# Kernel tuning notes

Measured on AMD Instinct MI355X. Metric: run time of the kernel, lower is better.

Reference implementation:

```python
import jax, jax.numpy as jnp
import numpy as np

DT = 0.03125                                   # ray-march step size
NSTEPS = int(np.ceil(2.0 * np.sqrt(3.0) / DT)) # enough steps to cross the [-1,1]^3 cube diagonal (=111)


def trilinear_sample(vol, pos):
    """vol: [C, D, Hv, Wv]; pos: [H, W, 3] xyz in [-1,1] (grid_sample convention,
    align_corners=True). Returns [C, H, W]."""
    D, Hv, Wv = vol.shape[1], vol.shape[2], vol.shape[3]

    def axis(g, n):
        g = jnp.clip((g + 1.0) * 0.5 * (n - 1), 0.0, n - 1.0)
        i0 = jnp.minimum(jnp.floor(g).astype(jnp.int32), n - 2)
        return i0, i0 + 1, (g - i0)[None]  # frac broadcast over channel dim

    x0, x1, fx = axis(pos[..., 0], Wv)
    y0, y1, fy = axis(pos[..., 1], Hv)
    z0, z1, fz = axis(pos[..., 2], D)

    def g(z, y, x):
        return vol[:, z, y, x]  # [C, H, W]

    c00 = g(z0, y0, x0) * (1 - fx) + g(z0, y0, x1) * fx
    c01 = g(z0, y1, x0) * (1 - fx) + g(z0, y1, x1) * fx
    c10 = g(z1, y0, x0) * (1 - fx) + g(z1, y0, x1) * fx
    c11 = g(z1, y1, x0) * (1 - fx) + g(z1, y1, x1) * fx
    c0 = c00 * (1 - fy) + c01 * fy
    c1 = c10 * (1 - fy) + c11 * fy
    return c0 * (1 - fz) + c1 * fz


def setup_inputs() -> dict:
    key = jax.random.key(0)
    B, H, W, D = 2, 256, 256, 128
    camrot = jnp.tile(jnp.eye(3, dtype=jnp.float32)[None], (B, 1, 1))
    campos = jnp.tile(jnp.array([[0.0, 0.0, -2.5]], dtype=jnp.float32), (B, 1))
    focal = jnp.full((B, 2), 300.0, dtype=jnp.float32)
    princpt = jnp.full((B, 2), 128.0, dtype=jnp.float32)
    ys, xs = jnp.meshgrid(jnp.arange(H, dtype=jnp.float32),
                          jnp.arange(W, dtype=jnp.float32), indexing='ij')
    pixelcoords = jnp.tile(jnp.stack([xs, ys], axis=-1)[None], (B, 1, 1, 1))
    volume = jax.random.uniform(key, (B, 4, D, D, D), dtype=jnp.float32)
    return dict(camrot=camrot, campos=campos, focal=focal, princpt=princpt,
                pixelcoords=pixelcoords, volume=volume)


def reference(camrot, campos, focal, princpt, pixelcoords, volume):
    # camera rays: pixel -> camera -> world (camrot^T applied, as in torch sum over dim=-2)
    raydir = (pixelcoords - princpt[:, None, None, :]) / focal[:, None, None, :]
    raydir = jnp.concatenate([raydir, jnp.ones_like(raydir[..., :1])], axis=-1)
    raydir = jnp.einsum('bij,bhwi->bhwj', camrot, raydir)
    raydir = raydir / jnp.sqrt(jnp.sum(raydir ** 2, axis=-1, keepdims=True))

    # ray-AABB intersection with [-1,1]^3 (no grad, as in torch.no_grad())
    t1 = (-1.0 - campos[:, None, None, :]) / raydir
    t2 = (1.0 - campos[:, None, None, :]) / raydir
    tmin = jnp.maximum(jnp.minimum(t1[..., 0], t2[..., 0]),
                       jnp.maximum(jnp.minimum(t1[..., 1], t2[..., 1]),
                                   jnp.minimum(t1[..., 2], t2[..., 2])))
    tmax = jnp.minimum(jnp.maximum(t1[..., 0], t2[..., 0]),
                       jnp.minimum(jnp.maximum(t1[..., 1], t2[..., 1]),
                                   jnp.maximum(t1[..., 2], t2[..., 2])))
    hit = tmin < tmax
    t0 = jax.lax.stop_gradient(jnp.maximum(jnp.where(hit, tmin, 0.0), 0.0))

    raypos = campos[:, None, None, :] + raydir * t0[..., None]  # [B,H,W,3]
    B, H, W = raypos.shape[:3]
    rayrgb = jnp.zeros((B, 3, H, W), raypos.dtype)
    rayalpha = jnp.zeros((B, 1, H, W), raypos.dtype)

    def step(carry, _):
        raypos, rayrgb, rayalpha = carry
        valid = jnp.all((raypos > -1.0) & (raypos < 1.0), axis=-1).astype(raypos.dtype)
        samp = jax.vmap(trilinear_sample)(volume, raypos)  # [B,4,H,W]
        contrib = (jnp.minimum(rayalpha + samp[:, 3:4] * DT, 1.0) - rayalpha) * valid[:, None]
        rayrgb = rayrgb + samp[:, :3] * contrib
        rayalpha = rayalpha + contrib
        raypos = raypos + raydir * DT
        return (raypos, rayrgb, rayalpha), None

    (_, rayrgb, rayalpha), _ = jax.lax.scan(step, (raypos, rayrgb, rayalpha),
                                            None, length=NSTEPS)
    return jnp.concatenate([rayrgb, rayalpha], axis=1)  # [B,4,H,W]
```

## Files before the change

kernel.cpp:

```cpp
#include <hip/hip_runtime.h>
#include <math.h>

#pragma clang fp contract(off)

#define DT 0.03125f
#define INV_DT 32.0f
#define NSTEPS 111

#if defined(__has_builtin)
#if __has_builtin(__builtin_amdgcn_udot4)
#define HAVE_UDOT4 1
#endif
#endif

__device__ __forceinline__ unsigned udot4(unsigned a, unsigned b) {
#ifdef HAVE_UDOT4
    return __builtin_amdgcn_udot4(a, b, 0u, false);
#else
    return (a & 0xffu) * (b & 0xffu)
         + ((a >> 8) & 0xffu) * ((b >> 8) & 0xffu)
         + ((a >> 16) & 0xffu) * ((b >> 16) & 0xffu)
         + ((a >> 24) & 0xffu) * ((b >> 24) & 0xffu);
#endif
}

typedef unsigned u32x4 __attribute__((ext_vector_type(4)));


__device__ __forceinline__ unsigned q8(float v) {
    return __float2uint_rn(fminf(fmaxf(v, 0.0f), 1.0f) * 255.0f);
}

template <int DD>
__global__ __launch_bounds__(256) void repack_u8x4_rowshare_kernel(
        const float* __restrict__ vol, uint4* __restrict__ out, long spatial) {
    constexpr int D = DD;
    constexpr int TPR = D / 4;
    constexpr int R = 1024 / D;
    constexpr int ZS = D * D;

    int t = threadIdx.x;
    long b = blockIdx.y;
    long s_base = (long)blockIdx.x << 10;
    int z = (int)(s_base / ZS);
    int rem = (int)(s_base - (long)z * ZS);
    int y0 = rem / D;
    int yl = t / TPR;
    int x0 = (t - yl * TPR) * 4;

    const float* base = vol + b * 4 * spatial + (long)z * ZS;

    __shared__ unsigned stage[4][R + 1][TPR];
    #pragma unroll
    for (int ci = 0; ci < 4; ++ci) {
        const float* p = base + (long)ci * spatial + (y0 + yl) * D + x0;
        float4 v = *(const float4*)p;
        stage[ci][yl][x0 >> 2] =
            q8(v.x) | (q8(v.y) << 8) | (q8(v.z) << 16) | (q8(v.w) << 24);
    }
    if (t < TPR) {
        int ye = y0 + R; if (ye > D - 1) ye = D - 1;
        #pragma unroll
        for (int ci = 0; ci < 4; ++ci) {
            const float* p = base + (long)ci * spatial + ye * D + t * 4;
            float4 v = *(const float4*)p;
            stage[ci][R][t] =
                q8(v.x) | (q8(v.y) << 8) | (q8(v.z) << 16) | (q8(v.w) << 24);
        }
    }
    __syncthreads();

    int w = x0 >> 2;
    bool last = (x0 + 4 >= D);
    uint4 e[4];
    #pragma unroll
    for (int ci = 0; ci < 4; ++ci) {
        unsigned wA0 = stage[ci][yl][w];
        unsigned wB0 = stage[ci][yl + 1][w];
        unsigned a4 = last ? (wA0 >> 24) : (stage[ci][yl][w + 1] & 0xffu);
        unsigned b4 = last ? (wB0 >> 24) : (stage[ci][yl + 1][w + 1] & 0xffu);
        unsigned a[5] = {wA0 & 0xffu, (wA0 >> 8) & 0xffu,
                         (wA0 >> 16) & 0xffu, wA0 >> 24, a4};
        unsigned bb[5] = {wB0 & 0xffu, (wB0 >> 8) & 0xffu,
                          (wB0 >> 16) & 0xffu, wB0 >> 24, b4};
        #pragma unroll
        for (int k = 0; k < 4; ++k) {
            ((unsigned*)&e[k])[ci] =
                a[k] | (a[k + 1] << 8) | (bb[k] << 16) | (bb[k + 1] << 24);
        }
    }

    __shared__ uint4 lds[4 * 257];
    #pragma unroll
    for (int j = 0; j < 4; ++j) lds[j * 257 + t] = e[j];
    __syncthreads();
    uint4* o = out + b * spatial + ((long)blockIdx.x << 10);
    #pragma unroll
    for (int k = 0; k < 4; ++k) {
        o[k * 256 + t] = lds[(t & 3) * 257 + k * 64 + (t >> 2)];
    }
}

__global__ __launch_bounds__(256) void repack_u8x4_lds_kernel(
        const float* __restrict__ vol, uint4* __restrict__ out,
        long spatial, int D) {
    long chunk = (long)blockIdx.x * 256 + threadIdx.x;
    long b = blockIdx.y;
    long s = chunk << 2;
    int zs = D * D;
    int z = (int)(s / zs);
    int rem = (int)(s - (long)z * zs);
    int y = rem / D;
    int x0 = rem - y * D;
    int y1 = (y < D - 1) ? y + 1 : y;
    bool last = (x0 + 4 >= D);

    const float* base = vol + b * 4 * spatial;
    uint4 e[4];
    #pragma unroll
    for (int ci = 0; ci < 4; ++ci) {
        const float* pa = base + (long)ci * spatial + (long)z * zs + y * D + x0;
        const float* pb = base + (long)ci * spatial + (long)z * zs + y1 * D + x0;
        float4 va = *(const float4*)pa;
        float4 vb = *(const float4*)pb;
        float na_sh = __shfl_down(va.x, 1, 64);
        float nb_sh = __shfl_down(vb.x, 1, 64);
        float na = last ? va.w : na_sh;
        float nb = last ? vb.w : nb_sh;
        float ra[5] = {va.x, va.y, va.z, va.w, na};
        float rb[5] = {vb.x, vb.y, vb.z, vb.w, nb};
        #pragma unroll
        for (int k = 0; k < 4; ++k) {
            unsigned d = q8(ra[k]) | (q8(ra[k + 1]) << 8) |
                         (q8(rb[k]) << 16) | (q8(rb[k + 1]) << 24);
            ((unsigned*)&e[k])[ci] = d;
        }
    }

    __shared__ uint4 lds[4 * 257];
    int t = threadIdx.x;
    #pragma unroll
    for (int j = 0; j < 4; ++j) lds[j * 257 + t] = e[j];
    __syncthreads();
    uint4* o = out + b * spatial + ((long)blockIdx.x << 10);
    #pragma unroll
    for (int k = 0; k < 4; ++k) {
        o[k * 256 + t] = lds[(t & 3) * 257 + k * 64 + (t >> 2)];
    }
}

__global__ __launch_bounds__(256) void repack_u8x4_kernel(const float* __restrict__ vol,
                                                          uint4* __restrict__ out,
                                                          long spatial, int D) {
    long chunk = (long)blockIdx.x * blockDim.x + threadIdx.x;
    long nchunks = spatial >> 2;
    if (chunk >= nchunks) return;
    long b = blockIdx.y;
    long s = chunk << 2;
    int zs = D * D;
    int z = (int)(s / zs);
    int rem = (int)(s - (long)z * zs);
    int y = rem / D;
    int x0 = rem - y * D;
    int y1 = (y < D - 1) ? y + 1 : y;

    const float* base = vol + b * 4 * spatial;
    uint4 e[4];
    #pragma unroll
    for (int ci = 0; ci < 4; ++ci) {
        const float* pa = base + (long)ci * spatial + (long)z * zs + y * D + x0;
        const float* pb = base + (long)ci * spatial + (long)z * zs + y1 * D + x0;
        float4 va = *(const float4*)pa;
        float4 vb = *(const float4*)pb;
        bool last = (x0 + 4 >= D);
        float na = last ? pa[3] : pa[4];
        float nb = last ? pb[3] : pb[4];
        float ra[5] = {va.x, va.y, va.z, va.w, na};
        float rb[5] = {vb.x, vb.y, vb.z, vb.w, nb};
        #pragma unroll
        for (int k = 0; k < 4; ++k) {
            unsigned d = q8(ra[k]) | (q8(ra[k + 1]) << 8) |
                         (q8(rb[k]) << 16) | (q8(rb[k + 1]) << 24);
            ((unsigned*)&e[k])[ci] = d;
        }
    }
    uint4* o = out + b * spatial + s;
    o[0] = e[0]; o[1] = e[1]; o[2] = e[2]; o[3] = e[3];
}

__global__ __launch_bounds__(256) void repack_u8_kernel(const float* __restrict__ vol,
                                                        uint4* __restrict__ out,
                                                        long total, long spatial, int D) {
    long idx = (long)blockIdx.x * blockDim.x + threadIdx.x;
    if (idx >= total) return;
    long b = idx / spatial;
    long s = idx - b * spatial;
    int zs = D * D;
    int z = (int)(s / zs);
    int rem = (int)(s - (long)z * zs);
    int y = rem / D;
    int x = rem - y * D;
    int x1 = (x < D - 1) ? x + 1 : x;
    int y1 = (y < D - 1) ? y + 1 : y;
    const float* base = vol + b * 4 * spatial;
    uint4 e;
    #pragma unroll
    for (int ci = 0; ci < 4; ++ci) {
        const float* p = base + (long)ci * spatial + (long)z * zs;
        unsigned d = q8(p[y * D + x]) | (q8(p[y * D + x1]) << 8) |
                     (q8(p[y1 * D + x]) << 16) | (q8(p[y1 * D + x1]) << 24);
        ((unsigned*)&e)[ci] = d;
    }
    out[idx] = e;
}


struct Ray {
    float posx, posy, posz;
    float stx, sty, stz;
    int n;
};

__device__ __forceinline__ Ray ray_setup(const float* __restrict__ camrot,
                                         const float* __restrict__ campos,
                                         const float* __restrict__ focal,
                                         const float* __restrict__ princpt,
                                         const float* __restrict__ pixelcoords,
                                         int b, int y, int x, int H, int W) {
#pragma clang fp contract(off)
    long pidx = (((long)b * H + y) * W + x) * 2;
    float px = pixelcoords[pidx];
    float py = pixelcoords[pidx + 1];
    const float* R = camrot + b * 9;
    float cpx = campos[b * 3 + 0], cpy = campos[b * 3 + 1], cpz = campos[b * 3 + 2];
    float flx = focal[b * 2 + 0], fly = focal[b * 2 + 1];
    float prx = princpt[b * 2 + 0], pry = princpt[b * 2 + 1];

    float rx = (px - prx) / flx;
    float ry = (py - pry) / fly;
    float rz = 1.0f;
    float dx = R[0] * rx + R[3] * ry + R[6] * rz;
    float dy = R[1] * rx + R[4] * ry + R[7] * rz;
    float dz = R[2] * rx + R[5] * ry + R[8] * rz;
    float ss = dx * dx;
    ss = ss + dy * dy;
    ss = ss + dz * dz;
    float nrm = sqrtf(ss);
    dx = dx / nrm; dy = dy / nrm; dz = dz / nrm;

    float t1x = (-1.0f - cpx) / dx, t2x = (1.0f - cpx) / dx;
    float t1y = (-1.0f - cpy) / dy, t2y = (1.0f - cpy) / dy;
    float t1z = (-1.0f - cpz) / dz, t2z = (1.0f - cpz) / dz;
    float tmin = fmaxf(fminf(t1x, t2x), fmaxf(fminf(t1y, t2y), fminf(t1z, t2z)));
    float tmax = fminf(fmaxf(t1x, t2x), fminf(fmaxf(t1y, t2y), fmaxf(t1z, t2z)));
    bool hit = tmin < tmax;
    float t0 = fmaxf(hit ? tmin : 0.0f, 0.0f);

    Ray r;
    r.posx = cpx + dx * t0;
    r.posy = cpy + dy * t0;
    r.posz = cpz + dz * t0;
    r.stx = dx * DT; r.sty = dy * DT; r.stz = dz * DT;

    float span = (tmax - t0) * INV_DT + 4.0f;
    span = fminf(span, (float)NSTEPS);
    r.n = (hit && span > 0.0f) ? (int)span : 0;
    return r;
}


#define ISTEP(C, u)                                                            \
    {                                                                          \
        bool inside = (ipx > -1.0f) && (ipx < 1.0f) && (ipy > -1.0f) &&        \
                      (ipy < 1.0f) && (ipz > -1.0f) && (ipz < 1.0f);           \
        C.m##u = inside ? 1.0f : 0.0f;                                         \
        float gx, gy, gz;                                                      \
        {                                                                      \
            _Pragma("clang fp contract(fast)")                                 \
            gx = ipx * gsc + gsc;                                              \
            gy = ipy * gsc + gsc;                                              \
            gz = ipz * gsc + gsc;                                              \
        }                                                                      \
        int ix = (int)gx; ix = min(max(ix, 0), D - 2);                         \
        int iy = (int)gy; iy = min(max(iy, 0), D - 2);                         \
        int iz = (int)gz; iz = min(max(iz, 0), D - 2);                         \
        float fx = gx - (float)ix;                                             \
        float fy = gy - (float)iy;                                             \
        C.fz##u = gz - (float)iz;                                              \
        unsigned wx1 = (unsigned)(int)(fx * 255.0f + 0.5f);                    \
        unsigned wy1 = (unsigned)(int)(fy * 255.0f + 0.5f);                    \
        unsigned wx0 = 255u - wx1, wy0 = 255u - wy1;                           \
        unsigned p00 = ((wx0 * wy0 + 128u) >> 8) & 0xffu;                      \
        unsigned p10 = ((wx1 * wy0 + 128u) >> 8) & 0xffu;                      \
        unsigned p01 = ((wx0 * wy1 + 128u) >> 8) & 0xffu;                      \
        unsigned p11 = ((wx1 * wy1 + 128u) >> 8) & 0xffu;                      \
        C.wp##u = p00 | (p10 << 8) | (p01 << 16) | (p11 << 24);                \
        unsigned voff = (unsigned)((iz * zs + iy * D + ix) << 4);              \
        asm volatile("global_load_dwordx4 %0, %2, %3\n\t"                      \
                     "global_load_dwordx4 %1, %2, %4"                          \
                     : "=&v"(C.A##u), "=&v"(C.B##u)                            \
                     : "v"(voff), "s"(vp), "s"(vpb)                            \
                     : "memory");                                              \
        ipx = ipx + stx; ipy = ipy + sty; ipz = ipz + stz;                     \
    }

#define CSTEP(C, u)                                                            \
    {                                                                          \
        unsigned wp = C.wp##u;                                                 \
        float rA = (float)udot4(C.A##u[0], wp), rB = (float)udot4(C.B##u[0], wp); \
        float gA = (float)udot4(C.A##u[1], wp), gB = (float)udot4(C.B##u[1], wp); \
        float bA = (float)udot4(C.A##u[2], wp), bB = (float)udot4(C.B##u[2], wp); \
        float sA = (float)udot4(C.A##u[3], wp), sB = (float)udot4(C.B##u[3], wp); \
        float fz = C.fz##u;                                                    \
        float rS, gS, bS, sw;                                                  \
        {                                                                      \
            _Pragma("clang fp contract(fast)")                                 \
            rS = rA + fz * (rB - rA);                                          \
            gS = gA + fz * (gB - gA);                                          \
            bS = bA + fz * (bB - bA);                                          \
            sw = (sA + fz * (sB - sA)) * inv;                                  \
        }                                                                      \
        float contrib = (fminf(alpha + sw * DT, 1.0f) - alpha) * C.m##u;       \
        {                                                                      \
            _Pragma("clang fp contract(fast)")                                 \
            accr = accr + rS * contrib;                                        \
            accg = accg + gS * contrib;                                        \
            accb = accb + bS * contrib;                                        \
        }                                                                      \
        alpha = alpha + contrib;                                               \
        pxx = pxx + stx; pyy = pyy + sty; pzz = pzz + stz;                     \
    }

#define ISSUE_CHUNK(C)   { ISTEP(C, 0) ISTEP(C, 1) ISTEP(C, 2) ISTEP(C, 3) }
#define CONSUME_CHUNK(C) { CSTEP(C, 0) CSTEP(C, 1) CSTEP(C, 2) CSTEP(C, 3) }

#define WAIT_VM15                                                              \
    asm volatile("s_waitcnt vmcnt(15)" ::: "memory");                          \
    __builtin_amdgcn_sched_barrier(0);
#define WAIT_VM0                                                               \
    asm volatile("s_waitcnt vmcnt(0)" ::: "memory");                           \
    __builtin_amdgcn_sched_barrier(0);

#define MARCH_TAIL_STEP                                                        \
    {                                                                          \
        bool inside = (pxx > -1.0f) && (pxx < 1.0f) && (pyy > -1.0f) &&        \
                      (pyy < 1.0f) && (pzz > -1.0f) && (pzz < 1.0f);           \
        float m = inside ? 1.0f : 0.0f;                                        \
        float gx, gy, gz;                                                      \
        {                                                                      \
            _Pragma("clang fp contract(fast)")                                 \
            gx = pxx * gsc + gsc;                                              \
            gy = pyy * gsc + gsc;                                              \
            gz = pzz * gsc + gsc;                                              \
        }                                                                      \
        int ix = (int)gx; ix = min(max(ix, 0), D - 2);                         \
        int iy = (int)gy; iy = min(max(iy, 0), D - 2);                         \
        int iz = (int)gz; iz = min(max(iz, 0), D - 2);                         \
        float fx = gx - (float)ix;                                             \
        float fy = gy - (float)iy;                                             \
        float fz = gz - (float)iz;                                             \
        unsigned wx1 = (unsigned)(int)(fx * 255.0f + 0.5f);                    \
        unsigned wy1 = (unsigned)(int)(fy * 255.0f + 0.5f);                    \
        unsigned wx0 = 255u - wx1, wy0 = 255u - wy1;                           \
        unsigned p00 = ((wx0 * wy0 + 128u) >> 8) & 0xffu;                      \
        unsigned p10 = ((wx1 * wy0 + 128u) >> 8) & 0xffu;                      \
        unsigned p01 = ((wx0 * wy1 + 128u) >> 8) & 0xffu;                      \
        unsigned p11 = ((wx1 * wy1 + 128u) >> 8) & 0xffu;                      \
        unsigned wp = p00 | (p10 << 8) | (p01 << 16) | (p11 << 24);            \
        const u32x4* p_ = vp + (iz * zs + iy * D + ix);                        \
        u32x4 A = p_[0];                                                       \
        u32x4 Bv = p_[zs];                                                     \
        float rA = (float)udot4(A[0], wp), rB = (float)udot4(Bv[0], wp);       \
        float gA = (float)udot4(A[1], wp), gB = (float)udot4(Bv[1], wp);       \
        float bA = (float)udot4(A[2], wp), bB = (float)udot4(Bv[2], wp);       \
        float sA = (float)udot4(A[3], wp), sB = (float)udot4(Bv[3], wp);       \
        float rS, gS, bS, sw;                                                  \
        {                                                                      \
            _Pragma("clang fp contract(fast)")                                 \
            rS = rA + fz * (rB - rA);                                          \
            gS = gA + fz * (gB - gA);                                          \
            bS = bA + fz * (bB - bA);                                          \
            sw = (sA + fz * (sB - sA)) * inv;                                  \
        }                                                                      \
        float contrib = (fminf(alpha + sw * DT, 1.0f) - alpha) * m;            \
        {                                                                      \
            _Pragma("clang fp contract(fast)")                                 \
            accr = accr + rS * contrib;                                        \
            accg = accg + gS * contrib;                                        \
            accb = accb + bS * contrib;                                        \
        }                                                                      \
        alpha = alpha + contrib;                                               \
        pxx = pxx + stx; pyy = pyy + sty; pzz = pzz + stz;                     \
    }

struct Chunk {
    u32x4 A0, A1, A2, A3, B0, B1, B2, B3;
    unsigned wp0, wp1, wp2, wp3;
    float fz0, fz1, fz2, fz3;
    float m0, m1, m2, m3;
};

template <int DD>
__global__ __launch_bounds__(256, 2) void raymarch_dot_kernel(
        const float* __restrict__ camrot, const float* __restrict__ campos,
        const float* __restrict__ focal, const float* __restrict__ princpt,
        const float* __restrict__ pixelcoords, const uint4* __restrict__ vol,
        float* __restrict__ out, int B, int H, int W, int Drt) {
#pragma clang fp contract(off)
    const int D = (DD > 0) ? DD : Drt;
    int x = blockIdx.x * 16 + threadIdx.x;
    int y = blockIdx.y * 16 + threadIdx.y;
    int b = blockIdx.z;
    if (x >= W || y >= H) return;

    Ray r = ray_setup(camrot, campos, focal, princpt, pixelcoords, b, y, x, H, W);

    float accr = 0.0f, accg = 0.0f, accb = 0.0f, alpha = 0.0f;
    const float gsc = 0.5f * (float)(D - 1);
    const float inv = 1.0f / (255.0f * 255.0f);
    const int zs = D * D;
    const u32x4* vp = (const u32x4*)vol + (long)b * ((long)zs * D);
    const u32x4* vpb = vp + zs;
    float pxx = r.posx, pyy = r.posy, pzz = r.posz;
    float ipx = r.posx, ipy = r.posy, ipz = r.posz;
    float stx = r.stx, sty = r.sty, stz = r.stz;

    int nb = r.n & ~3;
    int chunks = nb >> 2;

    WAIT_VM0;

    Chunk c0, c1, c2;
    ISSUE_CHUNK(c0);
    ISSUE_CHUNK(c1);
    ISSUE_CHUNK(c2);

    int k = 0;
    if (chunks > 0) {
        for (;;) {
            WAIT_VM15;
            CONSUME_CHUNK(c0);
            ++k;
            if (alpha == 1.0f || k >= chunks) break;
            ISSUE_CHUNK(c0);
            WAIT_VM15;
            CONSUME_CHUNK(c1);
            ++k;
            if (alpha == 1.0f || k >= chunks) break;
            ISSUE_CHUNK(c1);
            WAIT_VM15;
            CONSUME_CHUNK(c2);
            ++k;
            if (alpha == 1.0f || k >= chunks) break;
            ISSUE_CHUNK(c2);
        }
    }
    WAIT_VM0;

    if (alpha != 1.0f) {
        for (int s = k << 2; s < r.n; ++s) { MARCH_TAIL_STEP; }
    }

    long hw = (long)H * W;
    long o = (long)b * 4 * hw + (long)y * W + x;
    out[o] = accr * inv;
    out[o + hw] = accg * inv;
    out[o + 2 * hw] = accb * inv;
    out[o + 3 * hw] = alpha;
}


__global__ __launch_bounds__(256) void raymarch_simple_kernel(
        const float* __restrict__ camrot, const float* __restrict__ campos,
        const float* __restrict__ focal, const float* __restrict__ princpt,
        const float* __restrict__ pixelcoords, const float* __restrict__ vol,
        float* __restrict__ out, int B, int H, int W, int D) {
#pragma clang fp contract(off)
    int x = blockIdx.x * blockDim.x + threadIdx.x;
    int y = blockIdx.y * blockDim.y + threadIdx.y;
    int b = blockIdx.z;
    if (x >= W || y >= H) return;

    Ray r = ray_setup(camrot, campos, focal, princpt, pixelcoords, b, y, x, H, W);

    float accr = 0.0f, accg = 0.0f, accb = 0.0f, alpha = 0.0f;
    float gmax = (float)(D - 1);
    long spatial = (long)D * D * D;
    long zstride = (long)D * D;
    const float* vb = vol + (long)b * 4 * spatial;
    float pxx = r.posx, pyy = r.posy, pzz = r.posz;

    for (int s = 0; s < r.n; ++s) {
        bool inside = (pxx > -1.0f) && (pxx < 1.0f) && (pyy > -1.0f) &&
                      (pyy < 1.0f) && (pzz > -1.0f) && (pzz < 1.0f);
        float m = inside ? 1.0f : 0.0f;
        float gx = fminf(fmaxf((pxx + 1.0f) * 0.5f * gmax, 0.0f), gmax);
        float gy = fminf(fmaxf((pyy + 1.0f) * 0.5f * gmax, 0.0f), gmax);
        float gz = fminf(fmaxf((pzz + 1.0f) * 0.5f * gmax, 0.0f), gmax);
        int ix0 = (int)floorf(gx); if (ix0 > D - 2) ix0 = D - 2;
        int iy0 = (int)floorf(gy); if (iy0 > D - 2) iy0 = D - 2;
        int iz0 = (int)floorf(gz); if (iz0 > D - 2) iz0 = D - 2;
        float fx = gx - (float)ix0;
        float fy = gy - (float)iy0;
        float fz = gz - (float)iz0;

        long s000 = (long)iz0 * zstride + (long)iy0 * D + ix0;
        float c[8][4];
        const long offs[8] = {s000, s000 + 1, s000 + D, s000 + D + 1,
                              s000 + zstride, s000 + zstride + 1,
                              s000 + zstride + D, s000 + zstride + D + 1};
        #pragma unroll
        for (int k = 0; k < 8; ++k) {
            c[k][0] = vb[offs[k]];
            c[k][1] = vb[offs[k] + spatial];
            c[k][2] = vb[offs[k] + 2 * spatial];
            c[k][3] = vb[offs[k] + 3 * spatial];
        }
        float wa = 1.0f - fx, wb = 1.0f - fy, wc = 1.0f - fz;
        float samp[4];
        #pragma unroll
        for (int ci = 0; ci < 4; ++ci) {
            float c00 = c[0][ci] * wa + c[1][ci] * fx;
            float c01 = c[2][ci] * wa + c[3][ci] * fx;
            float c10 = c[4][ci] * wa + c[5][ci] * fx;
            float c11 = c[6][ci] * wa + c[7][ci] * fx;
            float c0 = c00 * wb + c01 * fy;
            float c1 = c10 * wb + c11 * fy;
            samp[ci] = c0 * wc + c1 * fz;
        }
        float contrib = (fminf(alpha + samp[3] * DT, 1.0f) - alpha) * m;
        accr = accr + samp[0] * contrib;
        accg = accg + samp[1] * contrib;
        accb = accb + samp[2] * contrib;
        alpha = alpha + contrib;
        pxx = pxx + r.stx; pyy = pyy + r.sty; pzz = pzz + r.stz;
    }

    long hw = (long)H * W;
    long o = (long)b * 4 * hw + (long)y * W + x;
    out[o] = accr;
    out[o + hw] = accg;
    out[o + 2 * hw] = accb;
    out[o + 3 * hw] = alpha;
}

extern "C" void kernel_launch(void* const* d_in, const int* in_sizes, int n_in,
                              void* d_out, int out_size, void* d_ws, size_t ws_size,
                              hipStream_t stream) {
    const float* camrot = (const float*)d_in[0];
    const float* campos = (const float*)d_in[1];
    const float* focal = (const float*)d_in[2];
    const float* princpt = (const float*)d_in[3];
    const float* pixelcoords = (const float*)d_in[4];
    const float* volume = (const float*)d_in[5];
    float* out = (float*)d_out;

    int B = in_sizes[0] / 9;
    long spatial = (long)in_sizes[5] / (B * 4);
    int D = (int)lround(cbrt((double)spatial));
    while ((long)D * D * D > spatial) D--;
    while ((long)(D + 1) * (D + 1) * (D + 1) <= spatial) D++;
    long hw = (long)in_sizes[4] / (B * 2);
    int H = (int)lround(sqrt((double)hw));
    int W = H;

    size_t vol_bytes = (size_t)B * spatial * sizeof(uint4);

    if (ws_size >= vol_bytes && D >= 2) {
        uint4* vol8 = (uint4*)d_ws;
        long nchunks = spatial >> 2;
        bool rowshare_ok = (D == 128) && ((nchunks % 256) == 0);
        bool lds_ok = ((D & 3) == 0) && ((64 % (D / 4)) == 0) &&
                      ((nchunks % 256) == 0);
        if (rowshare_ok) {
            dim3 rgrd((unsigned)(nchunks / 256), B, 1);
            repack_u8x4_rowshare_kernel<128><<<rgrd, dim3(256), 0, stream>>>(
                volume, vol8, spatial);
        } else if (lds_ok) {
            dim3 rgrd((unsigned)(nchunks / 256), B, 1);
            repack_u8x4_lds_kernel<<<rgrd, dim3(256), 0, stream>>>(volume, vol8,
                                                                   spatial, D);
        } else if ((D & 3) == 0) {
            dim3 rgrd((unsigned)((nchunks + 255) / 256), B, 1);
            repack_u8x4_kernel<<<rgrd, dim3(256), 0, stream>>>(volume, vol8, spatial, D);
        } else {
            long total = (long)B * spatial;
            repack_u8_kernel<<<dim3((unsigned)((total + 255) / 256)), dim3(256), 0,
                               stream>>>(volume, vol8, total, spatial, D);
        }
        dim3 blk(16, 16, 1);
        dim3 grd((W + 15) / 16, (H + 15) / 16, B);
        if (D == 128) {
            raymarch_dot_kernel<128><<<grd, blk, 0, stream>>>(
                camrot, campos, focal, princpt, pixelcoords, vol8, out, B, H, W, D);
        } else {
            raymarch_dot_kernel<0><<<grd, blk, 0, stream>>>(
                camrot, campos, focal, princpt, pixelcoords, vol8, out, B, H, W, D);
        }
    } else {
        dim3 blk(16, 16, 1);
        dim3 grd((W + 15) / 16, (H + 15) / 16, B);
        raymarch_simple_kernel<<<grd, blk, 0, stream>>>(camrot, campos, focal, princpt,
                                                        pixelcoords, volume,
                                                        out, B, H, W, D);
    }
}
```

Baseline: 137.4 us.

## Overlap batch-1 volume repack with batch-0 ray marching in a fused kernel

For D=128 and B=2, the launches are split per batch. Batch 0 is repacked first. A fused kernel then marches batch 0 and repacks batch 1 in different blocks. A final kernel marches batch 1. This lets the memory-bound repack of the second volume run alongside compute-heavy marching, instead of as a full serial pass before all marching. The cost is an extra launch and a fused kernel whose register budget is set by the march body, which may hurt occupancy for the repack blocks.

```diff
diff --git a/kernel.cpp b/kernel.cpp
--- a/kernel.cpp
+++ b/kernel.cpp
@@ -32,23 +32,22 @@
 }
 
 template <int DD>
-__global__ __launch_bounds__(256) void repack_u8x4_rowshare_kernel(
-        const float* __restrict__ vol, uint4* __restrict__ out, long spatial) {
+__device__ __forceinline__ void repack_rowshare_body(
+        const float* __restrict__ vol, uint4* __restrict__ out, long spatial,
+        int chunkblk, int b, int t) {
     constexpr int D = DD;
     constexpr int TPR = D / 4;
     constexpr int R = 1024 / D;
     constexpr int ZS = D * D;
 
-    int t = threadIdx.x;
-    long b = blockIdx.y;
-    long s_base = (long)blockIdx.x << 10;
+    long s_base = (long)chunkblk << 10;
     int z = (int)(s_base / ZS);
     int rem = (int)(s_base - (long)z * ZS);
     int y0 = rem / D;
     int yl = t / TPR;
     int x0 = (t - yl * TPR) * 4;
 
-    const float* base = vol + b * 4 * spatial + (long)z * ZS;
+    const float* base = vol + (long)b * 4 * spatial + (long)z * ZS;
 
     __shared__ unsigned stage[4][R + 1][TPR];
     #pragma unroll
@@ -94,11 +93,19 @@
     #pragma unroll
     for (int j = 0; j < 4; ++j) lds[j * 257 + t] = e[j];
     __syncthreads();
-    uint4* o = out + b * spatial + ((long)blockIdx.x << 10);
+    uint4* o = out + (long)b * spatial + ((long)chunkblk << 10);
     #pragma unroll
     for (int k = 0; k < 4; ++k) {
         o[k * 256 + t] = lds[(t & 3) * 257 + k * 64 + (t >> 2)];
     }
+}
+
+template <int DD>
+__global__ __launch_bounds__(256) void repack_u8x4_rowshare_kernel(
+        const float* __restrict__ vol, uint4* __restrict__ out, long spatial,
+        int bbase) {
+    repack_rowshare_body<DD>(vol, out, spatial, blockIdx.x,
+                             bbase + blockIdx.y, threadIdx.x);
 }
 
 __global__ __launch_bounds__(256) void repack_u8x4_lds_kernel(
@@ -401,16 +408,16 @@
 };
 
 template <int DD>
-__global__ __launch_bounds__(256, 2) void raymarch_dot_kernel(
+__device__ __forceinline__ void march_body(
         const float* __restrict__ camrot, const float* __restrict__ campos,
         const float* __restrict__ focal, const float* __restrict__ princpt,
         const float* __restrict__ pixelcoords, const uint4* __restrict__ vol,
-        float* __restrict__ out, int B, int H, int W, int Drt) {
+        float* __restrict__ out, int H, int W, int Drt,
+        int bx, int by, int b, int tx, int ty) {
 #pragma clang fp contract(off)
     const int D = (DD > 0) ? DD : Drt;
-    int x = blockIdx.x * 16 + threadIdx.x;
-    int y = blockIdx.y * 16 + threadIdx.y;
-    int b = blockIdx.z;
+    int x = bx * 16 + tx;
+    int y = by * 16 + ty;
     if (x >= W || y >= H) return;
 
     Ray r = ray_setup(camrot, campos, focal, princpt, pixelcoords, b, y, x, H, W);
@@ -469,6 +476,35 @@
     out[o + 3 * hw] = alpha;
 }
 
+template <int DD>
+__global__ __launch_bounds__(256, 2) void raymarch_dot_kernel(
+        const float* __restrict__ camrot, const float* __restrict__ campos,
+        const float* __restrict__ focal, const float* __restrict__ princpt,
+        const float* __restrict__ pixelcoords, const uint4* __restrict__ vol,
+        float* __restrict__ out, int H, int W, int Drt, int bbase) {
+    march_body<DD>(camrot, campos, focal, princpt, pixelcoords, vol, out,
+                   H, W, Drt, blockIdx.x, blockIdx.y, bbase + blockIdx.z,
+                   threadIdx.x & 15, threadIdx.x >> 4);
+}
+
+template <int DD>
+__global__ __launch_bounds__(256, 2) void fused_march0_repack1_kernel(
+        const float* __restrict__ camrot, const float* __restrict__ campos,
+        const float* __restrict__ focal, const float* __restrict__ princpt,
+        const float* __restrict__ pixelcoords, const float* __restrict__ volf,
+        uint4* __restrict__ vol8, float* __restrict__ out,
+        int H, int W, long spatial, int march_blocks, int mtx) {
+    int bid = blockIdx.x;
+    if (bid < march_blocks) {
+        march_body<DD>(camrot, campos, focal, princpt, pixelcoords, vol8, out,
+                       H, W, DD, bid % mtx, bid / mtx, 0,
+                       threadIdx.x & 15, threadIdx.x >> 4);
+    } else {
+        repack_rowshare_body<DD>(volf, vol8, spatial, bid - march_blocks, 1,
+                                 threadIdx.x);
+    }
+}
+
 
 __global__ __launch_bounds__(256) void raymarch_simple_kernel(
         const float* __restrict__ camrot, const float* __restrict__ campos,
@@ -570,12 +606,29 @@
         uint4* vol8 = (uint4*)d_ws;
         long nchunks = spatial >> 2;
         bool rowshare_ok = (D == 128) && ((nchunks % 256) == 0);
+        int mtx = (W + 15) / 16, mty = (H + 15) / 16;
+
+        if (rowshare_ok && B == 2) {
+            unsigned rblk = (unsigned)(nchunks / 256);
+            int march_blocks = mtx * mty;
+            repack_u8x4_rowshare_kernel<128><<<dim3(rblk, 1), dim3(256), 0,
+                                               stream>>>(volume, vol8, spatial, 0);
+            fused_march0_repack1_kernel<128><<<dim3(rblk + march_blocks), dim3(256),
+                                               0, stream>>>(
+                camrot, campos, focal, princpt, pixelcoords, volume, vol8, out,
+                H, W, spatial, march_blocks, mtx);
+            raymarch_dot_kernel<128><<<dim3(mtx, mty, 1), dim3(256), 0, stream>>>(
+                camrot, campos, focal, princpt, pixelcoords, vol8, out,
+                H, W, D, 1);
+            return;
+        }
+
         bool lds_ok = ((D & 3) == 0) && ((64 % (D / 4)) == 0) &&
                       ((nchunks % 256) == 0);
         if (rowshare_ok) {
             dim3 rgrd((unsigned)(nchunks / 256), B, 1);
             repack_u8x4_rowshare_kernel<128><<<rgrd, dim3(256), 0, stream>>>(
-                volume, vol8, spatial);
+                volume, vol8, spatial, 0);
         } else if (lds_ok) {
             dim3 rgrd((unsigned)(nchunks / 256), B, 1);
             repack_u8x4_lds_kernel<<<rgrd, dim3(256), 0, stream>>>(volume, vol8,
@@ -588,14 +641,13 @@
             repack_u8_kernel<<<dim3((unsigned)((total + 255) / 256)), dim3(256), 0,
                                stream>>>(volume, vol8, total, spatial, D);
         }
-        dim3 blk(16, 16, 1);
-        dim3 grd((W + 15) / 16, (H + 15) / 16, B);
+        dim3 grd(mtx, mty, B);
         if (D == 128) {
-            raymarch_dot_kernel<128><<<grd, blk, 0, stream>>>(
-                camrot, campos, focal, princpt, pixelcoords, vol8, out, B, H, W, D);
+            raymarch_dot_kernel<128><<<grd, dim3(256), 0, stream>>>(
+                camrot, campos, focal, princpt, pixelcoords, vol8, out, H, W, D, 0);
         } else {
-            raymarch_dot_kernel<0><<<grd, blk, 0, stream>>>(
-                camrot, campos, focal, princpt, pixelcoords, vol8, out, B, H, W, D);
+            raymarch_dot_kernel<0><<<grd, dim3(256), 0, stream>>>(
+                camrot, campos, focal, princpt, pixelcoords, vol8, out, H, W, D, 0);
         }
     } else {
         dim3 blk(16, 16, 1);
```

Measured after the change: 142.1 us. 1.03x slower.
